# Kernel tuning notes

Hardware: AMD Instinct MI355X
Metric: run time of the kernel (lower is better)

The kernel has to match this reference:

```python
import jax, jax.numpy as jnp
import numpy as np


def log_g(x):
    # log of g(x) = where(x>=0, x+0.5, sigmoid(x))
    return jnp.where(x >= 0, jnp.log(jnp.maximum(x, 0.0) + 0.5), -jax.nn.softplus(-x))


def setup_inputs() -> dict:
    key = jax.random.key(0)
    k1, k2 = jax.random.split(key)
    B, S, D = 8, 8192, 512
    x = jax.random.normal(k1, (B, S, D), dtype=jnp.float32)
    # to_hidden_and_gate weight: [2*D, D] (orthogonal init in torch; gaussian ok for reference)
    W = jax.random.normal(k2, (2 * D, D), dtype=jnp.float32) / np.sqrt(D)
    return {"x": x, "W": W}


def reference(x, W):
    # x: [B, S, D], W: [2D, D]
    hg = jnp.einsum('bsd,ed->bse', x, W)  # [B, S, 2D]
    D = x.shape[-1]
    hidden, gate = hg[..., :D], hg[..., D:]

    # log-domain minGRU (Heinsen associative scan)
    log_coeffs = -jax.nn.softplus(gate)            # log(1 - z)
    log_z = -jax.nn.softplus(-gate)                # log(z)
    log_values = log_z + log_g(hidden)             # log(z * g(h~))

    a_star = jnp.cumsum(log_coeffs, axis=1)
    log_h = a_star + jax.lax.cumlogsumexp(log_values - a_star, axis=1)
    out = jnp.exp(log_h)                           # [B, S, D]

    next_prev_hidden = out[:, -1:]
    return out, next_prev_hidden
```

## Files before the change

### kernel.cpp

```cpp
#include <hip/hip_runtime.h>
#include <hip/hip_bf16.h>
#include <stdint.h>

typedef float f32x4 __attribute__((ext_vector_type(4)));
typedef __bf16 bf16x8 __attribute__((ext_vector_type(8)));
typedef unsigned short ushort8 __attribute__((ext_vector_type(8)));

#define NB 8
#define NS 8192
#define ND 512
#define NM (NB * NS)
#define NK 512

__device__ __forceinline__ unsigned short f2bf(float f) {
  unsigned u = __float_as_uint(f);
  u += 0x7FFFu + ((u >> 16) & 1u);
  return (unsigned short)(u >> 16);
}

__device__ __forceinline__ uint32_t cvtpk(float lo, float hi) {
  uint32_t r;
  asm("v_cvt_pk_bf16_f32 %0, %1, %2" : "=v"(r) : "v"(lo), "v"(hi));
  return r;
}

__global__ __launch_bounds__(256) void cvt_bf16(const float* __restrict__ src,
                                                unsigned short* __restrict__ dst,
                                                int n8) {
  int i = blockIdx.x * 256 + threadIdx.x;
  if (i >= n8) return;
  const float4* s = reinterpret_cast<const float4*>(src + (size_t)i * 8);
  float4 v0 = s[0], v1 = s[1];
  ushort8 o;
  o[0] = f2bf(v0.x); o[1] = f2bf(v0.y); o[2] = f2bf(v0.z); o[3] = f2bf(v0.w);
  o[4] = f2bf(v1.x); o[5] = f2bf(v1.y); o[6] = f2bf(v1.z); o[7] = f2bf(v1.w);
  *reinterpret_cast<ushort8*>(dst + (size_t)i * 8) = o;
}

__global__ __launch_bounds__(512) void gemm_ab(const float* __restrict__ x,
                                               const unsigned short* __restrict__ wb,
                                               uint32_t* __restrict__ pk,
                                               float* __restrict__ aggA,
                                               float* __restrict__ aggB) {
  __shared__ __align__(16) char lds[131072];

  const int tid = threadIdx.x;
  const int w = tid >> 6;
  const int lane = tid & 63;
  const int wm = w >> 2;
  const int wn = w & 3;
  const int orig = blockIdx.x;
  const int wg = (orig & 7) * 128 + (orig >> 3);
  const int mblk = wg >> 2;
  const int nblk = wg & 3;
  const int m0 = mblk * 256;
  const int n0 = nblk * 128;

  const int lrow = lane >> 3;
  const int aSrc = (((lane & 7) ^ lrow) << 2);
  const float* pAf[4];
#pragma unroll
  for (int g = 0; g < 4; ++g) {
    int row = (g * 8 + w) * 8 + lrow;
    pAf[g] = x + (size_t)(m0 + row) * NK + aSrc;
  }
  const int bSrc = (((lane & 7) ^ lrow) << 3);
  const unsigned short* pBf[4];
#pragma unroll
  for (int g = 0; g < 4; ++g) {
    int row = g * 64 + w * 8 + lrow;
    int e = (row < 128) ? (n0 + row) : (384 + n0 + row);
    pBf[g] = wb + (size_t)e * NK + bSrc;
  }

  auto stageA = [&](int buf, int kt) {
    char* base = lds + buf * 32768;
    const int ko = kt << 5;
#pragma unroll
    for (int g = 0; g < 4; ++g)
      __builtin_amdgcn_global_load_lds(
          (const __attribute__((address_space(1))) void*)(pAf[g] + ko),
          (__attribute__((address_space(3))) void*)(base + (g * 8 + w) * 1024),
          16, 0, 0);
  };
  auto stageB = [&](int buf, int pair) {
    char* base = lds + 65536 + buf * 32768;
    const int ko = pair << 6;
#pragma unroll
    for (int g = 0; g < 4; ++g)
      __builtin_amdgcn_global_load_lds(
          (const __attribute__((address_space(1))) void*)(pBf[g] + ko),
          (__attribute__((address_space(3))) void*)(base + g * 8192 + w * 1024),
          16, 0, 0);
  };

  const int fr = lane & 15;
  const int kg = lane >> 4;

  f32x4 acc[8][4];
#pragma unroll
  for (int i = 0; i < 8; ++i)
#pragma unroll
    for (int j = 0; j < 4; ++j) acc[i][j] = (f32x4)0.0f;

  stageA(0, 0);
  stageB(0, 0);
  __syncthreads();

#pragma unroll 1
  for (int kt = 0; kt < 16; ++kt) {
    const int cur = kt & 1;
    const int bp = (kt >> 1) & 1;
    if (kt < 15) stageA(cur ^ 1, kt + 1);
    if ((kt & 1) == 0 && kt < 14) stageB(bp ^ 1, (kt >> 1) + 1);

    const char* ldsA = lds + cur * 32768;
    const char* ldsB = lds + 65536 + bp * 32768;
    const int kk = (kt & 1) * 32;
    bf16x8 bfr[4];
#pragma unroll
    for (int n = 0; n < 4; ++n) {
      int rowB = ((n < 2) ? (wn * 32 + n * 16) : (128 + wn * 32 + (n - 2) * 16)) + fr;
      int sb = (kk * 2 + kg * 16) ^ ((rowB & 7) << 4);
      bfr[n] = *reinterpret_cast<const bf16x8*>(ldsB + rowB * 128 + sb);
    }
#pragma unroll
    for (int i = 0; i < 8; ++i) {
      int rowA = wm * 128 + i * 16 + fr;
      int s0 = (((2 * kg) ^ (fr & 7)) << 4);
      int s1 = (((2 * kg + 1) ^ (fr & 7)) << 4);
      f32x4 q0 = *reinterpret_cast<const f32x4*>(ldsA + rowA * 128 + s0);
      f32x4 q1 = *reinterpret_cast<const f32x4*>(ldsA + rowA * 128 + s1);
      uint4 u;
      u.x = cvtpk(q0[0], q0[1]);
      u.y = cvtpk(q0[2], q0[3]);
      u.z = cvtpk(q1[0], q1[1]);
      u.w = cvtpk(q1[2], q1[3]);
      bf16x8 af = *reinterpret_cast<bf16x8*>(&u);
#pragma unroll
      for (int j = 0; j < 4; ++j)
        acc[i][j] = __builtin_amdgcn_mfma_f32_16x16x32_bf16(af, bfr[j], acc[i][j], 0, 0, 0);
    }
    __syncthreads();
  }

  const float LOG2E = 1.44269504f;
#pragma unroll
  for (int n = 0; n < 2; ++n) {
    const int ch = wn * 32 + n * 16 + fr;
    float Am[8], Bm[8];
#pragma unroll
    for (int m = 0; m < 8; ++m) {
      float As = 1.0f, Bs = 0.0f;
#pragma unroll
      for (int r = 0; r < 4; ++r) {
        float hid = acc[m][n][r];
        float gat = acc[m][n + 2][r];
        float ex1 = __builtin_amdgcn_exp2f(gat * LOG2E);
        float a = __builtin_amdgcn_rcpf(1.0f + ex1);
        float z = 1.0f - a;
        float ex2 = __builtin_amdgcn_exp2f(-hid * LOG2E);
        float gn = __builtin_amdgcn_rcpf(1.0f + ex2);
        float g = (hid >= 0.0f) ? (hid + 0.5f) : gn;
        float bb = z * g;
        int row = wm * 128 + 16 * m + 4 * kg + r;
        pk[(size_t)(m0 + row) * ND + n0 + ch] =
            ((uint32_t)f2bf(bb) << 16) | (uint32_t)f2bf(a);
        Bs = fmaf(a, Bs, bb);
        As *= a;
      }
      Am[m] = As; Bm[m] = Bs;
    }
#pragma unroll
    for (int m = 0; m < 8; ++m) {
      float pA_ = __shfl_xor(Am[m], 16);
      float pB_ = __shfl_xor(Bm[m], 16);
      Bm[m] = (kg & 1) ? fmaf(Am[m], pB_, Bm[m]) : fmaf(pA_, Bm[m], pB_);
      Am[m] *= pA_;
      pA_ = __shfl_xor(Am[m], 32);
      pB_ = __shfl_xor(Bm[m], 32);
      Bm[m] = (kg & 2) ? fmaf(Am[m], pB_, Bm[m]) : fmaf(pA_, Bm[m], pB_);
      Am[m] *= pA_;
    }
    float As = Am[0], Bs = Bm[0];
#pragma unroll
    for (int m = 1; m < 8; ++m) { Bs = fmaf(Am[m], Bs, Bm[m]); As *= Am[m]; }
    if (kg == 0) {
      size_t o = (size_t)(mblk * 2 + wm) * ND + n0 + ch;
      aggA[o] = As;
      aggB[o] = Bs;
    }
  }
}

__global__ __launch_bounds__(256) void scan_pass2(const uint32_t* __restrict__ pk,
                                                  const float* __restrict__ aggA,
                                                  const float* __restrict__ aggB,
                                                  float* __restrict__ out,
                                                  float* __restrict__ nextp) {
  int bid = blockIdx.x;
  int b = bid >> 6;
  int c = bid & 63;
  int d2 = threadIdx.x;

  float h0 = 0.0f, h1 = 0.0f;
  for (int cc = 0; cc < c; ++cc) {
    int o = (b * 64 + cc) * ND + d2 * 2;
    float2 Aa = *reinterpret_cast<const float2*>(&aggA[o]);
    float2 Bb = *reinterpret_cast<const float2*>(&aggB[o]);
    h0 = fmaf(Aa.x, h0, Bb.x);
    h1 = fmaf(Aa.y, h1, Bb.y);
  }
  size_t base = (size_t)(b * NS + c * 128) * ND + d2 * 2;
#pragma unroll 4
  for (int t = 0; t < 128; ++t) {
    size_t idx = base + (size_t)t * ND;
    uint2 v = *reinterpret_cast<const uint2*>(pk + idx);
    float a0 = __uint_as_float(v.x << 16);
    float b0 = __uint_as_float(v.x & 0xffff0000u);
    float a1 = __uint_as_float(v.y << 16);
    float b1 = __uint_as_float(v.y & 0xffff0000u);
    h0 = fmaf(a0, h0, b0);
    h1 = fmaf(a1, h1, b1);
    *reinterpret_cast<float2*>(&out[idx]) = make_float2(h0, h1);
  }
  if (c == 63) {
    *reinterpret_cast<float2*>(&nextp[b * ND + d2 * 2]) = make_float2(h0, h1);
  }
}

extern "C" void kernel_launch(void* const* d_in, const int* in_sizes, int n_in,
                              void* d_out, int out_size, void* d_ws, size_t ws_size,
                              hipStream_t stream) {
  const float* x = (const float*)d_in[0];
  const float* W = (const float*)d_in[1];
  float* out = (float*)d_out;

  char* ws = (char*)d_ws;
  uint32_t* pk = (uint32_t*)ws;
  unsigned short* wbf = (unsigned short*)(ws + (size_t)128 * 1024 * 1024);
  float* aggA = (float*)(ws + (size_t)129 * 1024 * 1024);
  float* aggB = (float*)(ws + (size_t)130 * 1024 * 1024);
  float* nextp = out + (size_t)NM * ND;

  cvt_bf16<<<256, 256, 0, stream>>>(W, wbf, (1024 * NK) / 8);
  gemm_ab<<<1024, 512, 0, stream>>>(x, wbf, pk, aggA, aggB);
  scan_pass2<<<512, 256, 0, stream>>>(pk, aggA, aggB, out, nextp);
}
```

Baseline: 197.6 us.

## Fuse scan into GEMM epilogue with flag-chained cross-block carry propagation

Removes the separate scan pass. Each GEMM block keeps its packed (a, b) coefficients in registers and waits on its predecessor tile's flag for the incoming hidden state. It then publishes its own end state and flag, and writes the final outputs directly. This drops the bf16-packed intermediate buffer's global write and re-read, one kernel launch, and the serial prefix over chunk aggregates. In exchange it adds an inter-block serial dependency chain with spin waits, which relies on in-order block dispatch to avoid stalls or deadlock, and needs a memset of the flags each call.

```diff
diff --git a/kernel.cpp b/kernel.cpp
--- a/kernel.cpp
+++ b/kernel.cpp
@@ -37,11 +37,12 @@
   *reinterpret_cast<ushort8*>(dst + (size_t)i * 8) = o;
 }
 
-__global__ __launch_bounds__(512) void gemm_ab(const float* __restrict__ x,
-                                               const unsigned short* __restrict__ wb,
-                                               uint32_t* __restrict__ pk,
-                                               float* __restrict__ aggA,
-                                               float* __restrict__ aggB) {
+__global__ __launch_bounds__(512) void gemm_scan(const float* __restrict__ x,
+                                                 const unsigned short* __restrict__ wb,
+                                                 float* __restrict__ out,
+                                                 float* __restrict__ nextp,
+                                                 float* __restrict__ hbuf,
+                                                 int* __restrict__ flags) {
   __shared__ __align__(16) char lds[131072];
 
   const int tid = threadIdx.x;
@@ -145,10 +146,13 @@
   }
 
   const float LOG2E = 1.44269504f;
+  uint32_t pkw[2][8][4];
+  float sA[2][8], sB[2][8];
+  float gA[2][8], gB[2][8];
+  float cA[2], cB[2];
+
 #pragma unroll
   for (int n = 0; n < 2; ++n) {
-    const int ch = wn * 32 + n * 16 + fr;
-    float Am[8], Bm[8];
 #pragma unroll
     for (int m = 0; m < 8; ++m) {
       float As = 1.0f, Bs = 0.0f;
@@ -163,69 +167,90 @@
         float gn = __builtin_amdgcn_rcpf(1.0f + ex2);
         float g = (hid >= 0.0f) ? (hid + 0.5f) : gn;
         float bb = z * g;
-        int row = wm * 128 + 16 * m + 4 * kg + r;
-        pk[(size_t)(m0 + row) * ND + n0 + ch] =
-            ((uint32_t)f2bf(bb) << 16) | (uint32_t)f2bf(a);
+        pkw[n][m][r] = ((uint32_t)f2bf(bb) << 16) | (uint32_t)f2bf(a);
         Bs = fmaf(a, Bs, bb);
         As *= a;
       }
-      Am[m] = As; Bm[m] = Bs;
-    }
+      sA[n][m] = As; sB[n][m] = Bs;
+      float A_ = As, B_ = Bs;
+      float pA_ = __shfl_xor(A_, 16);
+      float pB_ = __shfl_xor(B_, 16);
+      B_ = (kg & 1) ? fmaf(A_, pB_, B_) : fmaf(pA_, B_, pB_);
+      A_ *= pA_;
+      pA_ = __shfl_xor(A_, 32);
+      pB_ = __shfl_xor(B_, 32);
+      B_ = (kg & 2) ? fmaf(A_, pB_, B_) : fmaf(pA_, B_, pB_);
+      A_ *= pA_;
+      gA[n][m] = A_; gB[n][m] = B_;
+    }
+    float As = gA[n][0], Bs = gB[n][0];
+#pragma unroll
+    for (int m = 1; m < 8; ++m) { Bs = fmaf(gA[n][m], Bs, gB[n][m]); As *= gA[n][m]; }
+    cA[n] = As; cB[n] = Bs;
+  }
+
+  float* aggL = reinterpret_cast<float*>(lds);
+  if (kg == 0) {
+#pragma unroll
+    for (int n = 0; n < 2; ++n) {
+      int ch = wn * 32 + n * 16 + fr;
+      aggL[(wm * 128 + ch) * 2]     = cA[n];
+      aggL[(wm * 128 + ch) * 2 + 1] = cB[n];
+    }
+  }
+  __syncthreads();
+
+  const int flagIdx = mblk * 4 + nblk;
+  const bool firstInSeq = ((mblk & 31) == 0);
+  if (!firstInSeq) {
+    while (__hip_atomic_load(&flags[flagIdx - 4], __ATOMIC_ACQUIRE,
+                             __HIP_MEMORY_SCOPE_AGENT) == 0)
+      __builtin_amdgcn_s_sleep(8);
+  }
+
+  float h0s[2], h1s[2], he[2];
+#pragma unroll
+  for (int n = 0; n < 2; ++n) {
+    int ch = wn * 32 + n * 16 + fr;
+    float h0 = firstInSeq ? 0.0f : hbuf[(size_t)(flagIdx - 4) * 128 + ch];
+    float A0 = aggL[(0 * 128 + ch) * 2], B0 = aggL[(0 * 128 + ch) * 2 + 1];
+    float A1 = aggL[(1 * 128 + ch) * 2], B1 = aggL[(1 * 128 + ch) * 2 + 1];
+    h0s[n] = h0;
+    h1s[n] = fmaf(A0, h0, B0);
+    he[n]  = fmaf(A1, h1s[n], B1);
+    if (wm == 1 && kg == 0) hbuf[(size_t)flagIdx * 128 + ch] = he[n];
+  }
+  __syncthreads();
+  if (tid == 0)
+    __hip_atomic_store(&flags[flagIdx], 1, __ATOMIC_RELEASE, __HIP_MEMORY_SCOPE_AGENT);
+
+#pragma unroll
+  for (int n = 0; n < 2; ++n) {
+    int ch = wn * 32 + n * 16 + fr;
+    int d = n0 + ch;
+    float h = (wm == 0) ? h0s[n] : h1s[n];
 #pragma unroll
     for (int m = 0; m < 8; ++m) {
-      float pA_ = __shfl_xor(Am[m], 16);
-      float pB_ = __shfl_xor(Bm[m], 16);
-      Bm[m] = (kg & 1) ? fmaf(Am[m], pB_, Bm[m]) : fmaf(pA_, Bm[m], pB_);
-      Am[m] *= pA_;
-      pA_ = __shfl_xor(Am[m], 32);
-      pB_ = __shfl_xor(Bm[m], 32);
-      Bm[m] = (kg & 2) ? fmaf(Am[m], pB_, Bm[m]) : fmaf(pA_, Bm[m], pB_);
-      Am[m] *= pA_;
-    }
-    float As = Am[0], Bs = Bm[0];
-#pragma unroll
-    for (int m = 1; m < 8; ++m) { Bs = fmaf(Am[m], Bs, Bm[m]); As *= Am[m]; }
-    if (kg == 0) {
-      size_t o = (size_t)(mblk * 2 + wm) * ND + n0 + ch;
-      aggA[o] = As;
-      aggB[o] = Bs;
-    }
-  }
-}
-
-__global__ __launch_bounds__(256) void scan_pass2(const uint32_t* __restrict__ pk,
-                                                  const float* __restrict__ aggA,
-                                                  const float* __restrict__ aggB,
-                                                  float* __restrict__ out,
-                                                  float* __restrict__ nextp) {
-  int bid = blockIdx.x;
-  int b = bid >> 6;
-  int c = bid & 63;
-  int d2 = threadIdx.x;
-
-  float h0 = 0.0f, h1 = 0.0f;
-  for (int cc = 0; cc < c; ++cc) {
-    int o = (b * 64 + cc) * ND + d2 * 2;
-    float2 Aa = *reinterpret_cast<const float2*>(&aggA[o]);
-    float2 Bb = *reinterpret_cast<const float2*>(&aggB[o]);
-    h0 = fmaf(Aa.x, h0, Bb.x);
-    h1 = fmaf(Aa.y, h1, Bb.y);
-  }
-  size_t base = (size_t)(b * NS + c * 128) * ND + d2 * 2;
-#pragma unroll 4
-  for (int t = 0; t < 128; ++t) {
-    size_t idx = base + (size_t)t * ND;
-    uint2 v = *reinterpret_cast<const uint2*>(pk + idx);
-    float a0 = __uint_as_float(v.x << 16);
-    float b0 = __uint_as_float(v.x & 0xffff0000u);
-    float a1 = __uint_as_float(v.y << 16);
-    float b1 = __uint_as_float(v.y & 0xffff0000u);
-    h0 = fmaf(a0, h0, b0);
-    h1 = fmaf(a1, h1, b1);
-    *reinterpret_cast<float2*>(&out[idx]) = make_float2(h0, h1);
-  }
-  if (c == 63) {
-    *reinterpret_cast<float2*>(&nextp[b * ND + d2 * 2]) = make_float2(h0, h1);
+      float hseg = h;
+#pragma unroll
+      for (int j = 0; j < 3; ++j) {
+        float aj = __shfl(sA[n][m], fr + j * 16);
+        float bj = __shfl(sB[n][m], fr + j * 16);
+        if (j < kg) hseg = fmaf(aj, hseg, bj);
+      }
+#pragma unroll
+      for (int r = 0; r < 4; ++r) {
+        uint32_t p = pkw[n][m][r];
+        float a  = __uint_as_float(p << 16);
+        float bb = __uint_as_float(p & 0xffff0000u);
+        hseg = fmaf(a, hseg, bb);
+        int row = wm * 128 + m * 16 + kg * 4 + r;
+        out[(size_t)(m0 + row) * ND + d] = hseg;
+      }
+      h = fmaf(gA[n][m], h, gB[n][m]);
+    }
+    if ((mblk & 31) == 31 && wm == 1 && kg == 0)
+      nextp[(mblk >> 5) * ND + d] = he[n];
   }
 }
 
@@ -237,13 +262,12 @@
   float* out = (float*)d_out;
 
   char* ws = (char*)d_ws;
-  uint32_t* pk = (uint32_t*)ws;
-  unsigned short* wbf = (unsigned short*)(ws + (size_t)128 * 1024 * 1024);
-  float* aggA = (float*)(ws + (size_t)129 * 1024 * 1024);
-  float* aggB = (float*)(ws + (size_t)130 * 1024 * 1024);
+  unsigned short* wbf = (unsigned short*)ws;
+  int* flags = (int*)(ws + (size_t)1 * 1024 * 1024);
+  float* hbuf = (float*)(ws + (size_t)1 * 1024 * 1024 + 65536);
   float* nextp = out + (size_t)NM * ND;
 
+  hipMemsetAsync(flags, 0, 1024 * sizeof(int), stream);
   cvt_bf16<<<256, 256, 0, stream>>>(W, wbf, (1024 * NK) / 8);
-  gemm_ab<<<1024, 512, 0, stream>>>(x, wbf, pk, aggA, aggB);
-  scan_pass2<<<512, 256, 0, stream>>>(pk, aggA, aggB, out, nextp);
-}
+  gemm_scan<<<1024, 512, 0, stream>>>(x, wbf, out, nextp, hbuf, flags);
+}
```

Measured after the change: 382.5 us. +93.5%, slower.
